# Optimization experiments

Hardware: AMD Instinct MI355X
Metric: run time of the kernel (lower is better)

## Reference

```python
import jax, jax.numpy as jnp
import numpy as np

G = 0.001
EPS = 1e-6


def setup_inputs() -> dict:
    key = jax.random.key(0)
    k1, k2 = jax.random.split(key)
    B, N, D = 8, 4096, 3
    q = jax.random.normal(k1, (B, N, D), dtype=jnp.float32)
    m = jax.random.uniform(k2, (N,), dtype=jnp.float32)
    return {"q": q, "m": m}


def reference(q, m):
    # q: (B, N, D), m: (N,)
    N = q.shape[-2]
    diff = q[:, :, None, :] - q[:, None, :, :]          # (B, N, N, D)
    dist = jnp.sqrt(jnp.sum(diff * diff, axis=-1) + EPS)  # (B, N, N)
    mass_matrix = m[:, None] * m[None, :]                # (N, N)
    V = -G * mass_matrix / dist                          # (B, N, N)
    # zero the diagonal (self-interaction), matching fill_(0.0)
    off_diag = 1.0 - jnp.eye(N, dtype=q.dtype)
    V = V * off_diag
    return jnp.sum(V, axis=(-1, -2)) / 2.0               # (B,)
```

## Files before the change

kernel.cpp:

```cpp
#include <hip/hip_runtime.h>

typedef float v4f __attribute__((ext_vector_type(4)));

#define BLK 256
#define IPT 4
#define TI (BLK * IPT)
#define TJ 64
#define JBT (TI / TJ)
#define G_CONST 0.001f
#define EPS_CONST 1e-6f

__global__ __launch_bounds__(BLK, 4)
void grav_kernel(const float* __restrict__ q, const float* __restrict__ m,
                 float* __restrict__ out, int N) {
  const int b   = blockIdx.z;
  const int tid = threadIdx.x;

  int rel = blockIdx.x;
  int a = 0;
  while (rel >= JBT * (a + 1)) { rel -= JBT * (a + 1); ++a; }
  const int jt   = rel;
  const bool diag = (jt >= JBT * a);
  const int i0 = a * TI;
  const int j0 = jt * TJ;

  __shared__ float txs[TJ], tys[TJ], tzs[TJ], ssj[TJ], msj[TJ];
  __shared__ float wsum[4];

  const float* qb = q + (size_t)b * N * 3;

  if (tid < TJ) {
    const int j = j0 + tid;
    const float x = qb[3 * j + 0];
    const float y = qb[3 * j + 1];
    const float z = qb[3 * j + 2];
    txs[tid] = -2.f * x;
    tys[tid] = -2.f * y;
    tzs[tid] = -2.f * z;
    ssj[tid] = fmaf(x, x, fmaf(y, y, z * z));
    msj[tid] = m[j];
  }

  float xi[IPT], yi[IPT], zi[IPT], se[IPT], mi[IPT];
#pragma unroll
  for (int s = 0; s < IPT; ++s) {
    const int i = i0 + s * BLK + tid;
    xi[s] = qb[3 * i + 0];
    yi[s] = qb[3 * i + 1];
    zi[s] = qb[3 * i + 2];
    se[s] = fmaf(xi[s], xi[s], fmaf(yi[s], yi[s], fmaf(zi[s], zi[s], EPS_CONST)));
    mi[s] = m[i];
  }

  __syncthreads();

  float acc[IPT] = {0.f, 0.f, 0.f, 0.f};

  if (diag) {
    for (int k = 0; k < TJ; k += 4) {
      const v4f tx = *(const v4f*)&txs[k];
      const v4f ty = *(const v4f*)&tys[k];
      const v4f tz = *(const v4f*)&tzs[k];
      const v4f sj = *(const v4f*)&ssj[k];
      const v4f mj = *(const v4f*)&msj[k];
#pragma unroll
      for (int s = 0; s < IPT; ++s) {
        const int i = i0 + s * BLK + tid;
#pragma unroll
        for (int u = 0; u < 4; ++u) {
          float t = se[s] + sj[u];
          t = fmaf(xi[s], tx[u], t);
          t = fmaf(yi[s], ty[u], t);
          t = fmaf(zi[s], tz[u], t);
          float ri = __builtin_amdgcn_rsqf(t);
          ri = (i == j0 + k + u) ? 0.f : ri;
          acc[s] = fmaf(mj[u], ri, acc[s]);
        }
      }
    }
  } else {
    for (int k = 0; k < TJ; k += 4) {
      const v4f tx = *(const v4f*)&txs[k];
      const v4f ty = *(const v4f*)&tys[k];
      const v4f tz = *(const v4f*)&tzs[k];
      const v4f sj = *(const v4f*)&ssj[k];
      const v4f mj = *(const v4f*)&msj[k];
#pragma unroll
      for (int s = 0; s < IPT; ++s) {
#pragma unroll
        for (int u = 0; u < 4; ++u) {
          float t = se[s] + sj[u];
          t = fmaf(xi[s], tx[u], t);
          t = fmaf(yi[s], ty[u], t);
          t = fmaf(zi[s], tz[u], t);
          acc[s] = fmaf(mj[u], __builtin_amdgcn_rsqf(t), acc[s]);
        }
      }
    }
  }

  float tsum = 0.f;
#pragma unroll
  for (int s = 0; s < IPT; ++s) tsum += mi[s] * acc[s];

#pragma unroll
  for (int off = 32; off > 0; off >>= 1) tsum += __shfl_down(tsum, off);
  const int wid  = tid >> 6;
  const int lane = tid & 63;
  if (lane == 0) wsum[wid] = tsum;
  __syncthreads();
  if (tid == 0) {
    const float s = (wsum[0] + wsum[1]) + (wsum[2] + wsum[3]);
    const float scale = diag ? (-0.5f * G_CONST) : (-G_CONST);
    atomicAdd(out + b, s * scale);
  }
}

extern "C" void kernel_launch(void* const* d_in, const int* in_sizes, int n_in,
                              void* d_out, int out_size, void* d_ws, size_t ws_size,
                              hipStream_t stream) {
  const float* q = (const float*)d_in[0];
  const float* m = (const float*)d_in[1];
  float* out = (float*)d_out;

  const int N = in_sizes[1];
  const int B = in_sizes[0] / (N * 3);

  hipMemsetAsync(out, 0, (size_t)out_size * sizeof(float), stream);

  const int nti = N / TI;
  const int bpb = JBT * nti * (nti + 1) / 2;
  dim3 grid(bpb, 1, B);
  grav_kernel<<<grid, BLK, 0, stream>>>(q, m, out, N);
}
```

Before: 31.29 us.

## Precompute j-side SoA data in a prep kernel and read it directly from global

Adds a prep kernel that writes -2x, -2y, -2z and |q|^2 per particle into a structure-of-arrays workspace. The main kernel then reads j-data straight from global/L1 with vector loads instead of staging it through shared memory, which removes the __syncthreads. A fallback path rebuilds the same values from raw q when no workspace is available. IPT drops from 4 to 2, which doubles the block count and cuts per-thread reuse, and the extra launch adds overhead.

```diff
diff --git a/kernel.cpp b/kernel.cpp
--- a/kernel.cpp
+++ b/kernel.cpp
@@ -3,16 +3,32 @@
 typedef float v4f __attribute__((ext_vector_type(4)));
 
 #define BLK 256
-#define IPT 4
+#define IPT 2
 #define TI (BLK * IPT)
 #define TJ 64
 #define JBT (TI / TJ)
 #define G_CONST 0.001f
 #define EPS_CONST 1e-6f
 
+__global__ void prep_kernel(const float* __restrict__ q, float* __restrict__ jd,
+                            int N, int B) {
+  const int idx = blockIdx.x * blockDim.x + threadIdx.x;
+  if (idx >= B * N) return;
+  const int b = idx / N, j = idx - b * N;
+  const float x = q[(size_t)b * N * 3 + 3 * j + 0];
+  const float y = q[(size_t)b * N * 3 + 3 * j + 1];
+  const float z = q[(size_t)b * N * 3 + 3 * j + 2];
+  float* base = jd + (size_t)b * 4 * N;
+  base[0 * N + j] = -2.f * x;
+  base[1 * N + j] = -2.f * y;
+  base[2 * N + j] = -2.f * z;
+  base[3 * N + j] = fmaf(x, x, fmaf(y, y, z * z));
+}
+
+template<bool PREP>
 __global__ __launch_bounds__(BLK, 4)
 void grav_kernel(const float* __restrict__ q, const float* __restrict__ m,
-                 float* __restrict__ out, int N) {
+                 const float* __restrict__ jd, float* __restrict__ out, int N) {
   const int b   = blockIdx.z;
   const int tid = threadIdx.x;
 
@@ -24,22 +40,9 @@
   const int i0 = a * TI;
   const int j0 = jt * TJ;
 
-  __shared__ float txs[TJ], tys[TJ], tzs[TJ], ssj[TJ], msj[TJ];
   __shared__ float wsum[4];
 
   const float* qb = q + (size_t)b * N * 3;
-
-  if (tid < TJ) {
-    const int j = j0 + tid;
-    const float x = qb[3 * j + 0];
-    const float y = qb[3 * j + 1];
-    const float z = qb[3 * j + 2];
-    txs[tid] = -2.f * x;
-    tys[tid] = -2.f * y;
-    tzs[tid] = -2.f * z;
-    ssj[tid] = fmaf(x, x, fmaf(y, y, z * z));
-    msj[tid] = m[j];
-  }
 
   float xi[IPT], yi[IPT], zi[IPT], se[IPT], mi[IPT];
 #pragma unroll
@@ -52,48 +55,58 @@
     mi[s] = m[i];
   }
 
-  __syncthreads();
+  const float* txp = jd + ((size_t)b * 4 + 0) * N;
+  const float* typ = jd + ((size_t)b * 4 + 1) * N;
+  const float* tzp = jd + ((size_t)b * 4 + 2) * N;
+  const float* sjp = jd + ((size_t)b * 4 + 3) * N;
 
-  float acc[IPT] = {0.f, 0.f, 0.f, 0.f};
+  float acc[IPT] = {};
 
-  if (diag) {
-    for (int k = 0; k < TJ; k += 4) {
-      const v4f tx = *(const v4f*)&txs[k];
-      const v4f ty = *(const v4f*)&tys[k];
-      const v4f tz = *(const v4f*)&tzs[k];
-      const v4f sj = *(const v4f*)&ssj[k];
-      const v4f mj = *(const v4f*)&msj[k];
+#pragma unroll 2
+  for (int k = j0; k < j0 + TJ; k += 4) {
+    v4f txv, tyv, tzv, sjv;
+    const v4f mjv = *(const v4f*)&m[k];
+    if (PREP) {
+      txv = *(const v4f*)&txp[k];
+      tyv = *(const v4f*)&typ[k];
+      tzv = *(const v4f*)&tzp[k];
+      sjv = *(const v4f*)&sjp[k];
+    } else {
+      const v4f q0 = *(const v4f*)&qb[3 * k + 0];
+      const v4f q1 = *(const v4f*)&qb[3 * k + 4];
+      const v4f q2 = *(const v4f*)&qb[3 * k + 8];
+      const v4f xj = {q0.x, q0.w, q1.z, q2.y};
+      const v4f yj = {q0.y, q1.x, q1.w, q2.z};
+      const v4f zj = {q0.z, q1.y, q2.x, q2.w};
+      txv = -2.f * xj; tyv = -2.f * yj; tzv = -2.f * zj;
+      sjv = xj * xj + yj * yj + zj * zj;
+    }
+
+    if (diag) {
 #pragma unroll
       for (int s = 0; s < IPT; ++s) {
         const int i = i0 + s * BLK + tid;
 #pragma unroll
         for (int u = 0; u < 4; ++u) {
-          float t = se[s] + sj[u];
-          t = fmaf(xi[s], tx[u], t);
-          t = fmaf(yi[s], ty[u], t);
-          t = fmaf(zi[s], tz[u], t);
+          float t = se[s] + sjv[u];
+          t = fmaf(xi[s], txv[u], t);
+          t = fmaf(yi[s], tyv[u], t);
+          t = fmaf(zi[s], tzv[u], t);
           float ri = __builtin_amdgcn_rsqf(t);
-          ri = (i == j0 + k + u) ? 0.f : ri;
-          acc[s] = fmaf(mj[u], ri, acc[s]);
+          ri = (i == k + u) ? 0.f : ri;
+          acc[s] = fmaf(mjv[u], ri, acc[s]);
         }
       }
-    }
-  } else {
-    for (int k = 0; k < TJ; k += 4) {
-      const v4f tx = *(const v4f*)&txs[k];
-      const v4f ty = *(const v4f*)&tys[k];
-      const v4f tz = *(const v4f*)&tzs[k];
-      const v4f sj = *(const v4f*)&ssj[k];
-      const v4f mj = *(const v4f*)&msj[k];
+    } else {
 #pragma unroll
       for (int s = 0; s < IPT; ++s) {
 #pragma unroll
         for (int u = 0; u < 4; ++u) {
-          float t = se[s] + sj[u];
-          t = fmaf(xi[s], tx[u], t);
-          t = fmaf(yi[s], ty[u], t);
-          t = fmaf(zi[s], tz[u], t);
-          acc[s] = fmaf(mj[u], __builtin_amdgcn_rsqf(t), acc[s]);
+          float t = se[s] + sjv[u];
+          t = fmaf(xi[s], txv[u], t);
+          t = fmaf(yi[s], tyv[u], t);
+          t = fmaf(zi[s], tzv[u], t);
+          acc[s] = fmaf(mjv[u], __builtin_amdgcn_rsqf(t), acc[s]);
         }
       }
     }
@@ -131,5 +144,13 @@
   const int nti = N / TI;
   const int bpb = JBT * nti * (nti + 1) / 2;
   dim3 grid(bpb, 1, B);
-  grav_kernel<<<grid, BLK, 0, stream>>>(q, m, out, N);
+
+  const size_t need = (size_t)B * 4 * N * sizeof(float);
+  if (ws_size >= need) {
+    float* jd = (float*)d_ws;
+    prep_kernel<<<(B * N + 255) / 256, 256, 0, stream>>>(q, jd, N, B);
+    grav_kernel<true><<<grid, BLK, 0, stream>>>(q, m, jd, out, N);
+  } else {
+    grav_kernel<false><<<grid, BLK, 0, stream>>>(q, m, nullptr, out, N);
+  }
 }
```

New measurement: 47.53 us. +51.9%, slower.
